# Kernel optimization log

Hardware: AMD Instinct MI355X
Metric: run time of the kernel (lower is better)

## Reference

```python
import jax, jax.numpy as jnp
import numpy as np

D = 1024
DK = 1024
B, S = 4, 2048

def setup_inputs() -> dict:
    key = jax.random.key(0)
    ks = jax.random.split(key, 7)
    x = jax.random.normal(ks[0], (B, S, D), dtype=jnp.float32)
    mask = jnp.zeros((B, S, S), dtype=jnp.float32)
    scale = 1.0 / np.sqrt(D)
    Wq = jax.random.normal(ks[1], (D, DK), dtype=jnp.float32) * scale
    bq = jax.random.normal(ks[2], (DK,), dtype=jnp.float32) * 0.01
    Wk = jax.random.normal(ks[3], (D, DK), dtype=jnp.float32) * scale
    bk = jax.random.normal(ks[4], (DK,), dtype=jnp.float32) * 0.01
    Wv = jax.random.normal(ks[5], (D, DK), dtype=jnp.float32) * scale
    bv = jax.random.normal(ks[6], (DK,), dtype=jnp.float32) * 0.01
    return {"x": x, "mask": mask, "Wq": Wq, "bq": bq, "Wk": Wk, "bk": bk, "Wv": Wv, "bv": bv}

def reference(x, mask, Wq, bq, Wk, bk, Wv, bv):
    # Q/K/V projections: [B,S,D] @ [D,DK] + bias -> [B,S,DK]
    Q = jnp.einsum('bsd,dk->bsk', x, Wq) + bq
    K = jnp.einsum('bsd,dk->bsk', x, Wk) + bk
    V = jnp.einsum('bsd,dk->bsk', x, Wv) + bv
    scale = 1.0 / jnp.sqrt(jnp.asarray(DK, dtype=Q.dtype))
    scores = jnp.einsum('bqk,bpk->bqp', Q, K) * scale + mask  # [B,S,S]
    attn = jax.nn.softmax(scores, axis=-1)
    return jnp.einsum('bqp,bpk->bqk', attn, V)
```

## Files before the change

### kernel.cpp

```cpp
#include <hip/hip_runtime.h>
#include <hip/hip_bf16.h>
#include <stdint.h>

typedef unsigned short u16;
typedef __attribute__((ext_vector_type(4))) unsigned short u16x4;
typedef __attribute__((ext_vector_type(8))) short short8;
typedef __attribute__((ext_vector_type(4))) float f32x4;

__device__ inline u16 f2b(float f) {
  uint32_t u = __builtin_bit_cast(uint32_t, f);
  u += 0x7fffu + ((u >> 16) & 1u);
  return (u16)(u >> 16);
}
__device__ inline float b2f(u16 b) {
  return __builtin_bit_cast(float, (uint32_t)b << 16);
}

__global__ __launch_bounds__(256) void prep(
    const float* __restrict__ x, u16* __restrict__ xb,
    const float* __restrict__ Wq, const float* __restrict__ Wk,
    const float* __restrict__ Wv, u16* __restrict__ wT,
    const float* __restrict__ bq, const float* __restrict__ bk,
    const float* __restrict__ bv, float* __restrict__ biasC,
    float* __restrict__ rowsum) {
  __shared__ float tl[32][33];
  const int b = blockIdx.x;
  const int t = threadIdx.x;
  if (b < 8192) {
    long i = ((long)b * 256 + t) * 4;
    float4 v = *(const float4*)(x + i);
    u16x4 o = { f2b(v.x), f2b(v.y), f2b(v.z), f2b(v.w) };
    *(u16x4*)(xb + i) = o;
  } else if (b < 8192 + 3072) {
    const int bb = b - 8192;
    const int z = bb >> 10;
    const int tile = bb & 1023;
    const float* in = z == 0 ? Wq : (z == 1 ? Wk : Wv);
    u16* o = wT + (long)z * 1024 * 1024;
    const int c0 = (tile & 31) * 32, r0 = (tile >> 5) * 32;
    const int tx = t & 31, ty = t >> 5;
#pragma unroll
    for (int j = 0; j < 32; j += 8)
      tl[ty + j][tx] = in[(long)(r0 + ty + j) * 1024 + c0 + tx];
    __syncthreads();
#pragma unroll
    for (int j = 0; j < 32; j += 8)
      o[(long)(c0 + ty + j) * 1024 + r0 + tx] = f2b(tl[tx][ty + j]);
  } else {
    const int i = (b - 8192 - 3072) * 256 + t;
    if (i < 3072)
      biasC[i] = i < 1024 ? bq[i] : (i < 2048 ? bk[i - 1024] : bv[i - 2048]);
    else if (i < 3072 + 8192)
      rowsum[i - 3072] = 0.0f;
  }
}

#define BM 128
#define BN 128
#define BK 64

__device__ inline void load_lds16(const void* g, void* l) {
  __builtin_amdgcn_global_load_lds((const __attribute__((address_space(1))) void*)g,
                                   (__attribute__((address_space(3))) void*)l, 16, 0, 0);
}

template <int MODE>
__global__ __launch_bounds__(256, 2) void gemm_bt(
    const u16* __restrict__ A, const u16* __restrict__ Bt, void* __restrict__ C,
    u16* __restrict__ vtOut,
    const float* __restrict__ bias, const float* __restrict__ rsum,
    const float* __restrict__ maskG,
    int K, int lda, int ldb, int ldc,
    long sA, long sB, long sC,
    float scale)
{
  const int z = blockIdx.z;
  A += z * sA;
  Bt += z * sB;
  const long cbase = z * sC;

  __shared__ __align__(16) u16 lA[BM * BK];
  __shared__ __align__(16) u16 lB[BN * BK];

  const int t = threadIdx.x;
  const int lane = t & 63;
  const int wave = t >> 6;
  const int wr = wave >> 1, wc = wave & 1;
  const int m0 = blockIdx.y * BM, n0 = blockIdx.x * BN;

  const int fr = lane & 15;
  const int q4 = lane >> 4;
  const int r0 = q4 * 4;

  float mpre[4][4][4];
  if (MODE == 2) {
    const float* mk = maskG + (long)z * 2048 * 2048;
#pragma unroll
    for (int i = 0; i < 4; i++)
#pragma unroll
      for (int j = 0; j < 4; j++) {
        const int row = m0 + wr * 64 + i * 16 + r0;
        const int col = n0 + wc * 64 + j * 16 + fr;
#pragma unroll
        for (int r = 0; r < 4; r++)
          mpre[i][j][r] = mk[(long)(row + r) * 2048 + col];
      }
#pragma unroll
    for (int i = 0; i < 4; i++)
#pragma unroll
      for (int j = 0; j < 4; j++)
#pragma unroll
        for (int r = 0; r < 4; r++)
          asm volatile("" : "+v"(mpre[i][j][r]));
  }

  const int srow = t >> 3;
  const int schunk = (t & 7) ^ (srow & 7);
  const u16* aS = A + (long)(m0 + srow) * lda + schunk * 8;
  const u16* bS = Bt + (long)(n0 + srow) * ldb + schunk * 8;

  f32x4 acc[4][4] = {};

  for (int k0 = 0; k0 < K; k0 += BK) {
    __syncthreads();
#pragma unroll
    for (int i = 0; i < 4; i++) {
      load_lds16(aS + k0 + (long)(i * 32) * lda, &lA[(i * 256 + t) * 8]);
      load_lds16(bS + k0 + (long)(i * 32) * ldb, &lB[(i * 256 + t) * 8]);
    }
    __syncthreads();
#pragma unroll
    for (int kk = 0; kk < 2; kk++) {
      const int ch = kk * 4 + q4;
      short8 aF[4], bF[4];
#pragma unroll
      for (int i = 0; i < 4; i++) {
        int row = wr * 64 + i * 16 + fr;
        aF[i] = *(const short8*)&lA[row * BK + ((ch ^ (row & 7)) * 8)];
      }
#pragma unroll
      for (int j = 0; j < 4; j++) {
        int row = wc * 64 + j * 16 + fr;
        bF[j] = *(const short8*)&lB[row * BK + ((ch ^ (row & 7)) * 8)];
      }
#pragma unroll
      for (int i = 0; i < 4; i++)
#pragma unroll
        for (int j = 0; j < 4; j++)
          acc[i][j] = __builtin_amdgcn_mfma_f32_16x16x32_bf16(aF[i], bF[j], acc[i][j], 0, 0, 0);
    }
  }

  if (MODE == 2) {
    u16* Pout = (u16*)C + cbase;
    float* rz = (float*)rsum + (long)z * 2048;
#pragma unroll
    for (int i = 0; i < 4; i++) {
      const int row = m0 + wr * 64 + i * 16 + r0;
      float rs[4] = {0.f, 0.f, 0.f, 0.f};
#pragma unroll
      for (int j = 0; j < 4; j++) {
        const int col = n0 + wc * 64 + j * 16 + fr;
#pragma unroll
        for (int r = 0; r < 4; r++) {
          float e = __expf(acc[i][j][r] * scale + mpre[i][j][r]);
          Pout[(long)(row + r) * ldc + col] = f2b(e);
          rs[r] += e;
        }
      }
#pragma unroll
      for (int r = 0; r < 4; r++) {
        float s = rs[r];
        s += __shfl_xor(s, 1); s += __shfl_xor(s, 2);
        s += __shfl_xor(s, 4); s += __shfl_xor(s, 8);
        if (fr == 0) atomicAdd(&rz[row + r], s);
      }
    }
  } else if (MODE == 0) {
#pragma unroll
    for (int i = 0; i < 4; i++) {
#pragma unroll
      for (int j = 0; j < 4; j++) {
        const int row = m0 + wr * 64 + i * 16 + r0;
        const int col = n0 + wc * 64 + j * 16 + fr;
        const float b = bias[col];
        if (col >= 2048) {
          u16x4 o = { f2b(acc[i][j][0] + b), f2b(acc[i][j][1] + b),
                      f2b(acc[i][j][2] + b), f2b(acc[i][j][3] + b) };
          *(u16x4*)(vtOut + (long)(col - 2048) * 8192 + row) = o;
        } else {
#pragma unroll
          for (int r = 0; r < 4; r++)
            ((u16*)C)[(long)(row + r) * ldc + col] = f2b(acc[i][j][r] + b);
        }
      }
    }
  } else {
    const float* lz = rsum + (long)z * 2048;
#pragma unroll
    for (int i = 0; i < 4; i++) {
      const int row = m0 + wr * 64 + i * 16 + r0;
      float inv[4];
#pragma unroll
      for (int r = 0; r < 4; r++) inv[r] = 1.0f / lz[row + r];
#pragma unroll
      for (int j = 0; j < 4; j++) {
        const int col = n0 + wc * 64 + j * 16 + fr;
#pragma unroll
        for (int r = 0; r < 4; r++)
          ((float*)C)[cbase + (long)(row + r) * ldc + col] = acc[i][j][r] * inv[r];
      }
    }
  }
}

extern "C" void kernel_launch(void* const* d_in, const int* in_sizes, int n_in,
                              void* d_out, int out_size, void* d_ws, size_t ws_size,
                              hipStream_t stream) {
  const float* x    = (const float*)d_in[0];
  const float* mask = (const float*)d_in[1];
  const float* Wq   = (const float*)d_in[2];
  const float* bq   = (const float*)d_in[3];
  const float* Wk   = (const float*)d_in[4];
  const float* bk   = (const float*)d_in[5];
  const float* Wv   = (const float*)d_in[6];
  const float* bv   = (const float*)d_in[7];
  float* out = (float*)d_out;

  char* w = (char*)d_ws;
  u16*   xb    = (u16*)(w);
  u16*   wT    = (u16*)(w + 16777216);
  float* biasC = (float*)(w + 23068672);
  u16*   QKV   = (u16*)(w + 23081088);
  u16*   Vt    = (u16*)(w + 73414016);
  u16*   Pp    = (u16*)(w + 90191232);
  float* rowsum= (float*)(w + 123745664);

  prep<<<8192 + 3072 + 44, 256, 0, stream>>>(x, xb, Wq, Wk, Wv, wT, bq, bk, bv, biasC, rowsum);

  gemm_bt<0><<<dim3(24, 64, 1), 256, 0, stream>>>(xb, wT, QKV, Vt, biasC, nullptr, nullptr,
      1024, 1024, 1024, 3072, 0, 0, 0, 1.0f);

  gemm_bt<2><<<dim3(16, 16, 4), 256, 0, stream>>>(QKV, QKV + 1024, Pp, nullptr, nullptr, rowsum,
      mask,
      1024, 3072, 3072, 2048,
      2048L * 3072, 2048L * 3072, 2048L * 2048, 0.03125f);

  gemm_bt<4><<<dim3(8, 16, 4), 256, 0, stream>>>(Pp, Vt, out, nullptr, nullptr, rowsum, nullptr,
      2048, 2048, 8192, 1024,
      2048L * 2048, 2048L, 2048L * 1024, 1.0f);
}
```

Before: 308.2 us.

## Use 256x256 double-buffered 8-wave GEMM with interleaved LDS prefetch for QKV and scores

Replaces the 128x128 single-buffered GEMM for the QKV projection and the QK^T scores with a 512-thread, 256x256-tile kernel. It double-buffers LDS and splits each K-tile into four quarter-stages, issuing global-to-LDS loads for the next tile while MFMAs run, with explicit barriers, waitcnts and setprio. The mask is now loaded in the epilogue instead of being prefetched into registers, which frees registers for the larger accumulator. The P·V GEMM keeps the old kernel. The larger tiles give fewer blocks (384 and 256), which risks underfilling the CUs, and the hand-written wait counts are fragile.

```diff
diff --git a/kernel.cpp b/kernel.cpp
--- a/kernel.cpp
+++ b/kernel.cpp
@@ -55,115 +55,151 @@
   }
 }
 
-#define BM 128
-#define BN 128
-#define BK 64
-
 __device__ inline void load_lds16(const void* g, void* l) {
   __builtin_amdgcn_global_load_lds((const __attribute__((address_space(1))) void*)g,
                                    (__attribute__((address_space(3))) void*)l, 16, 0, 0);
 }
 
+#define BAR  asm volatile("s_barrier" ::: "memory")
+#define LGK0 asm volatile("s_waitcnt lgkmcnt(0)" ::: "memory")
+#define VM4  asm volatile("s_waitcnt vmcnt(4)" ::: "memory")
+
+#define MM(IH, JH) do {                                                        \
+  __builtin_amdgcn_s_setprio(1);                                               \
+  _Pragma("unroll")                                                            \
+  for (int i_ = 0; i_ < 4; i_++)                                               \
+    _Pragma("unroll")                                                          \
+    for (int j_ = 0; j_ < 2; j_++)                                             \
+      _Pragma("unroll")                                                        \
+      for (int kk_ = 0; kk_ < 2; kk_++)                                        \
+        acc[(IH)*4 + i_][(JH)*2 + j_] = __builtin_amdgcn_mfma_f32_16x16x32_bf16( \
+            aF[i_][kk_], bF[j_][kk_], acc[(IH)*4 + i_][(JH)*2 + j_], 0, 0, 0); \
+  __builtin_amdgcn_s_setprio(0);                                               \
+} while (0)
+
 template <int MODE>
-__global__ __launch_bounds__(256, 2) void gemm_bt(
+__global__ __launch_bounds__(512, 1) void gemm8(
     const u16* __restrict__ A, const u16* __restrict__ Bt, void* __restrict__ C,
-    u16* __restrict__ vtOut,
-    const float* __restrict__ bias, const float* __restrict__ rsum,
-    const float* __restrict__ maskG,
+    u16* __restrict__ vtOut, const float* __restrict__ bias,
+    float* __restrict__ rsum, const float* __restrict__ maskG,
     int K, int lda, int ldb, int ldc,
-    long sA, long sB, long sC,
-    float scale)
+    long sA_, long sB_, long sC_, float scale)
 {
   const int z = blockIdx.z;
-  A += z * sA;
-  Bt += z * sB;
-  const long cbase = z * sC;
-
-  __shared__ __align__(16) u16 lA[BM * BK];
-  __shared__ __align__(16) u16 lB[BN * BK];
+  A += z * sA_;
+  Bt += z * sB_;
+  const long cbase = z * sC_;
+
+  __shared__ __align__(16) u16 sA[2][256 * 64];
+  __shared__ __align__(16) u16 sB[2][256 * 64];
 
   const int t = threadIdx.x;
-  const int lane = t & 63;
-  const int wave = t >> 6;
-  const int wr = wave >> 1, wc = wave & 1;
-  const int m0 = blockIdx.y * BM, n0 = blockIdx.x * BN;
-
-  const int fr = lane & 15;
-  const int q4 = lane >> 4;
-  const int r0 = q4 * 4;
-
-  float mpre[4][4][4];
+  const int lane = t & 63, wave = t >> 6;
+  const int wr = wave >> 2, wc = wave & 3;
+  const int fr = lane & 15, q4 = lane >> 4;
+  const int m0 = blockIdx.y * 256, n0 = blockIdx.x * 256;
+  const int nT = K / 64;
+
+  auto stA = [&](int half, int kt, int buf) {
+    if (kt >= nT) kt = 0;
+    const long ko = (long)kt * 64;
+#pragma unroll
+    for (int ii = 0; ii < 2; ii++) {
+      int c = ii * 512 + t;
+      int rr = c >> 3, slot = c & 7;
+      int row = (rr < 64) ? (half * 64 + rr) : (128 + half * 64 + rr - 64);
+      int gch = slot ^ (row & 7);
+      load_lds16(A + (long)(m0 + row) * lda + ko + gch * 8,
+                 &sA[buf][row * 64 + slot * 8]);
+    }
+  };
+  auto stB = [&](int half, int kt, int buf) {
+    if (kt >= nT) kt = 0;
+    const long ko = (long)kt * 64;
+#pragma unroll
+    for (int ii = 0; ii < 2; ii++) {
+      int c = ii * 512 + t;
+      int rr = c >> 3, slot = c & 7;
+      int row = (rr >> 5) * 64 + half * 32 + (rr & 31);
+      int gch = slot ^ (row & 7);
+      load_lds16(Bt + (long)(n0 + row) * ldb + ko + gch * 8,
+                 &sB[buf][row * 64 + slot * 8]);
+    }
+  };
+
+  short8 aF[4][2], bF[2][2];
+  f32x4 acc[8][4] = {};
+
+  auto rdA = [&](int half, int buf) {
+#pragma unroll
+    for (int i = 0; i < 4; i++) {
+      int row = wr * 128 + half * 64 + i * 16 + fr;
+#pragma unroll
+      for (int kk = 0; kk < 2; kk++) {
+        int ch = kk * 4 + q4;
+        aF[i][kk] = *(const short8*)&sA[buf][row * 64 + ((ch ^ (row & 7)) * 8)];
+      }
+    }
+  };
+  auto rdB = [&](int half, int buf) {
+#pragma unroll
+    for (int j = 0; j < 2; j++) {
+      int row = wc * 64 + half * 32 + j * 16 + fr;
+#pragma unroll
+      for (int kk = 0; kk < 2; kk++) {
+        int ch = kk * 4 + q4;
+        bF[j][kk] = *(const short8*)&sB[buf][row * 64 + ((ch ^ (row & 7)) * 8)];
+      }
+    }
+  };
+
+  stA(0, 0, 0); stB(0, 0, 0); stB(1, 0, 0); stA(1, 0, 0);
+  VM4; BAR;
+
+  const int nIt = nT / 2;
+#pragma unroll 1
+  for (int it = 0; it < nIt; ++it) {
+    const int kt = 2 * it;
+    rdA(0, 0); rdB(0, 0); stA(0, kt + 1, 1);
+    BAR; LGK0; MM(0, 0); VM4; BAR;
+    rdB(1, 0);            stB(0, kt + 1, 1);
+    BAR; LGK0; MM(0, 1); VM4; BAR;
+    rdA(1, 0);            stB(1, kt + 1, 1);
+    BAR; LGK0; MM(1, 1);      BAR;
+    rdB(0, 0);            stA(1, kt + 1, 1);
+    BAR; LGK0; MM(1, 0); VM4; BAR;
+    rdA(0, 1); rdB(0, 1); stA(0, kt + 2, 0);
+    BAR; LGK0; MM(0, 0); VM4; BAR;
+    rdB(1, 1);            stB(0, kt + 2, 0);
+    BAR; LGK0; MM(0, 1); VM4; BAR;
+    rdA(1, 1);            stB(1, kt + 2, 0);
+    BAR; LGK0; MM(1, 1);      BAR;
+    rdB(0, 1);            stA(1, kt + 2, 0);
+    BAR; LGK0; MM(1, 0); VM4; BAR;
+  }
+
   if (MODE == 2) {
     const float* mk = maskG + (long)z * 2048 * 2048;
-#pragma unroll
-    for (int i = 0; i < 4; i++)
-#pragma unroll
-      for (int j = 0; j < 4; j++) {
-        const int row = m0 + wr * 64 + i * 16 + r0;
-        const int col = n0 + wc * 64 + j * 16 + fr;
-#pragma unroll
-        for (int r = 0; r < 4; r++)
-          mpre[i][j][r] = mk[(long)(row + r) * 2048 + col];
-      }
-#pragma unroll
-    for (int i = 0; i < 4; i++)
-#pragma unroll
-      for (int j = 0; j < 4; j++)
-#pragma unroll
-        for (int r = 0; r < 4; r++)
-          asm volatile("" : "+v"(mpre[i][j][r]));
-  }
-
-  const int srow = t >> 3;
-  const int schunk = (t & 7) ^ (srow & 7);
-  const u16* aS = A + (long)(m0 + srow) * lda + schunk * 8;
-  const u16* bS = Bt + (long)(n0 + srow) * ldb + schunk * 8;
-
-  f32x4 acc[4][4] = {};
-
-  for (int k0 = 0; k0 < K; k0 += BK) {
-    __syncthreads();
-#pragma unroll
-    for (int i = 0; i < 4; i++) {
-      load_lds16(aS + k0 + (long)(i * 32) * lda, &lA[(i * 256 + t) * 8]);
-      load_lds16(bS + k0 + (long)(i * 32) * ldb, &lB[(i * 256 + t) * 8]);
-    }
-    __syncthreads();
-#pragma unroll
-    for (int kk = 0; kk < 2; kk++) {
-      const int ch = kk * 4 + q4;
-      short8 aF[4], bF[4];
-#pragma unroll
-      for (int i = 0; i < 4; i++) {
-        int row = wr * 64 + i * 16 + fr;
-        aF[i] = *(const short8*)&lA[row * BK + ((ch ^ (row & 7)) * 8)];
-      }
-#pragma unroll
-      for (int j = 0; j < 4; j++) {
-        int row = wc * 64 + j * 16 + fr;
-        bF[j] = *(const short8*)&lB[row * BK + ((ch ^ (row & 7)) * 8)];
-      }
-#pragma unroll
-      for (int i = 0; i < 4; i++)
-#pragma unroll
-        for (int j = 0; j < 4; j++)
-          acc[i][j] = __builtin_amdgcn_mfma_f32_16x16x32_bf16(aF[i], bF[j], acc[i][j], 0, 0, 0);
-    }
-  }
-
-  if (MODE == 2) {
     u16* Pout = (u16*)C + cbase;
-    float* rz = (float*)rsum + (long)z * 2048;
-#pragma unroll
-    for (int i = 0; i < 4; i++) {
-      const int row = m0 + wr * 64 + i * 16 + r0;
-      float rs[4] = {0.f, 0.f, 0.f, 0.f};
+    float* rz = rsum + (long)z * 2048;
+#pragma unroll
+    for (int i = 0; i < 8; i++) {
+      const int row = m0 + wr * 128 + i * 16 + q4 * 4;
+      float ml[4][4];
 #pragma unroll
       for (int j = 0; j < 4; j++) {
         const int col = n0 + wc * 64 + j * 16 + fr;
 #pragma unroll
+        for (int r = 0; r < 4; r++)
+          ml[j][r] = mk[(long)(row + r) * 2048 + col];
+      }
+      float rs[4] = {0.f, 0.f, 0.f, 0.f};
+#pragma unroll
+      for (int j = 0; j < 4; j++) {
+        const int col = n0 + wc * 64 + j * 16 + fr;
+#pragma unroll
         for (int r = 0; r < 4; r++) {
-          float e = __expf(acc[i][j][r] * scale + mpre[i][j][r]);
+          float e = __expf(acc[i][j][r] * scale + ml[j][r]);
           Pout[(long)(row + r) * ldc + col] = f2b(e);
           rs[r] += e;
         }
@@ -176,12 +212,12 @@
         if (fr == 0) atomicAdd(&rz[row + r], s);
       }
     }
-  } else if (MODE == 0) {
-#pragma unroll
-    for (int i = 0; i < 4; i++) {
+  } else {
+#pragma unroll
+    for (int i = 0; i < 8; i++) {
 #pragma unroll
       for (int j = 0; j < 4; j++) {
-        const int row = m0 + wr * 64 + i * 16 + r0;
+        const int row = m0 + wr * 128 + i * 16 + q4 * 4;
         const int col = n0 + wc * 64 + j * 16 + fr;
         const float b = bias[col];
         if (col >= 2048) {
@@ -195,21 +231,85 @@
         }
       }
     }
-  } else {
-    const float* lz = rsum + (long)z * 2048;
+  }
+}
+
+#define BM 128
+#define BN 128
+#define BK 64
+
+__global__ __launch_bounds__(256, 2) void gemm_pv(
+    const u16* __restrict__ A, const u16* __restrict__ Bt, float* __restrict__ C,
+    const float* __restrict__ rsum,
+    int K, int lda, int ldb, int ldc, long sA_, long sB_, long sC_)
+{
+  const int z = blockIdx.z;
+  A += z * sA_;
+  Bt += z * sB_;
+  const long cbase = z * sC_;
+
+  __shared__ __align__(16) u16 lA[BM * BK];
+  __shared__ __align__(16) u16 lB[BN * BK];
+
+  const int t = threadIdx.x;
+  const int lane = t & 63;
+  const int wave = t >> 6;
+  const int wr = wave >> 1, wc = wave & 1;
+  const int m0 = blockIdx.y * BM, n0 = blockIdx.x * BN;
+
+  const int srow = t >> 3;
+  const int schunk = (t & 7) ^ (srow & 7);
+  const u16* aS = A + (long)(m0 + srow) * lda + schunk * 8;
+  const u16* bS = Bt + (long)(n0 + srow) * ldb + schunk * 8;
+
+  f32x4 acc[4][4] = {};
+  const int fr = lane & 15;
+  const int q4 = lane >> 4;
+
+  for (int k0 = 0; k0 < K; k0 += BK) {
+    __syncthreads();
 #pragma unroll
     for (int i = 0; i < 4; i++) {
-      const int row = m0 + wr * 64 + i * 16 + r0;
-      float inv[4];
-#pragma unroll
-      for (int r = 0; r < 4; r++) inv[r] = 1.0f / lz[row + r];
+      load_lds16(aS + k0 + (long)(i * 32) * lda, &lA[(i * 256 + t) * 8]);
+      load_lds16(bS + k0 + (long)(i * 32) * ldb, &lB[(i * 256 + t) * 8]);
+    }
+    __syncthreads();
+#pragma unroll
+    for (int kk = 0; kk < 2; kk++) {
+      const int ch = kk * 4 + q4;
+      short8 aF[4], bF[4];
+#pragma unroll
+      for (int i = 0; i < 4; i++) {
+        int row = wr * 64 + i * 16 + fr;
+        aF[i] = *(const short8*)&lA[row * BK + ((ch ^ (row & 7)) * 8)];
+      }
 #pragma unroll
       for (int j = 0; j < 4; j++) {
-        const int col = n0 + wc * 64 + j * 16 + fr;
-#pragma unroll
-        for (int r = 0; r < 4; r++)
-          ((float*)C)[cbase + (long)(row + r) * ldc + col] = acc[i][j][r] * inv[r];
-      }
+        int row = wc * 64 + j * 16 + fr;
+        bF[j] = *(const short8*)&lB[row * BK + ((ch ^ (row & 7)) * 8)];
+      }
+#pragma unroll
+      for (int i = 0; i < 4; i++)
+#pragma unroll
+        for (int j = 0; j < 4; j++)
+          acc[i][j] = __builtin_amdgcn_mfma_f32_16x16x32_bf16(aF[i], bF[j], acc[i][j], 0, 0, 0);
+    }
+  }
+
+  const int r0 = q4 * 4;
+  const float* lz = rsum + (long)z * 2048;
+#pragma unroll
+  for (int i = 0; i < 4; i++) {
+    const int row = m0 + wr * 64 + i * 16 + r0;
+    float inv[4];
+#pragma unroll
+    for (int r = 0; r < 4; r++) inv[r] = 1.0f / lz[row + r];
+#pragma unroll
+    for (int j = 0; j < 4; j++) {
+      const int col = n0 + wc * 64 + j * 16 + fr;
+#pragma unroll
+      for (int r = 0; r < 4; r++)
+        C[cbase + (long)(row + r) * ldc + col] = acc[i][j][r] * inv[r];
     }
   }
 }
@@ -238,15 +338,15 @@
 
   prep<<<8192 + 3072 + 44, 256, 0, stream>>>(x, xb, Wq, Wk, Wv, wT, bq, bk, bv, biasC, rowsum);
 
-  gemm_bt<0><<<dim3(24, 64, 1), 256, 0, stream>>>(xb, wT, QKV, Vt, biasC, nullptr, nullptr,
+  gemm8<0><<<dim3(12, 32, 1), 512, 0, stream>>>(xb, wT, QKV, Vt, biasC, nullptr, nullptr,
       1024, 1024, 1024, 3072, 0, 0, 0, 1.0f);
 
-  gemm_bt<2><<<dim3(16, 16, 4), 256, 0, stream>>>(QKV, QKV + 1024, Pp, nullptr, nullptr, rowsum,
+  gemm8<2><<<dim3(8, 8, 4), 512, 0, stream>>>(QKV, QKV + 1024, Pp, nullptr, nullptr, rowsum,
       mask,
       1024, 3072, 3072, 2048,
       2048L * 3072, 2048L * 3072, 2048L * 2048, 0.03125f);
 
-  gemm_bt<4><<<dim3(8, 16, 4), 256, 0, stream>>>(Pp, Vt, out, nullptr, nullptr, rowsum, nullptr,
+  gemm_pv<<<dim3(8, 16, 4), 256, 0, stream>>>(Pp, Vt, out, rowsum,
       2048, 2048, 8192, 1024,
-      2048L * 2048, 2048L, 2048L * 1024, 1.0f);
-}
+      2048L * 2048, 2048L, 2048L * 1024);
+}
```

New measurement: 313.2 us. About the same (+1.6%).

## Fuse prep and three GEMM stages into one persistent kernel with grid barriers

Applied to the files above, without the earlier changes.

Replaces the four separate launches (prep, QKV projection, score+exp, PV) with a single persistent kernel of 512 blocks. Blocks loop over each stage's tiles and synchronise through atomic-counter grid barriers, with a memset to reset the counters. Mask loading in the score stage moves from a register prefetch before the GEMM loop to per-row loads in the epilogue. This removes launch gaps and frees registers, but adds barrier spin cost and makes tiles run in fixed waves, so stages whose tile count does not divide evenly by 512 leave some blocks idle.

```diff
diff --git a/kernel.cpp b/kernel.cpp
--- a/kernel.cpp
+++ b/kernel.cpp
@@ -12,107 +12,42 @@
   u += 0x7fffu + ((u >> 16) & 1u);
   return (u16)(u >> 16);
 }
-__device__ inline float b2f(u16 b) {
-  return __builtin_bit_cast(float, (uint32_t)b << 16);
-}
-
-__global__ __launch_bounds__(256) void prep(
-    const float* __restrict__ x, u16* __restrict__ xb,
-    const float* __restrict__ Wq, const float* __restrict__ Wk,
-    const float* __restrict__ Wv, u16* __restrict__ wT,
-    const float* __restrict__ bq, const float* __restrict__ bk,
-    const float* __restrict__ bv, float* __restrict__ biasC,
-    float* __restrict__ rowsum) {
-  __shared__ float tl[32][33];
-  const int b = blockIdx.x;
-  const int t = threadIdx.x;
-  if (b < 8192) {
-    long i = ((long)b * 256 + t) * 4;
-    float4 v = *(const float4*)(x + i);
-    u16x4 o = { f2b(v.x), f2b(v.y), f2b(v.z), f2b(v.w) };
-    *(u16x4*)(xb + i) = o;
-  } else if (b < 8192 + 3072) {
-    const int bb = b - 8192;
-    const int z = bb >> 10;
-    const int tile = bb & 1023;
-    const float* in = z == 0 ? Wq : (z == 1 ? Wk : Wv);
-    u16* o = wT + (long)z * 1024 * 1024;
-    const int c0 = (tile & 31) * 32, r0 = (tile >> 5) * 32;
-    const int tx = t & 31, ty = t >> 5;
-#pragma unroll
-    for (int j = 0; j < 32; j += 8)
-      tl[ty + j][tx] = in[(long)(r0 + ty + j) * 1024 + c0 + tx];
-    __syncthreads();
-#pragma unroll
-    for (int j = 0; j < 32; j += 8)
-      o[(long)(c0 + ty + j) * 1024 + r0 + tx] = f2b(tl[tx][ty + j]);
-  } else {
-    const int i = (b - 8192 - 3072) * 256 + t;
-    if (i < 3072)
-      biasC[i] = i < 1024 ? bq[i] : (i < 2048 ? bk[i - 1024] : bv[i - 2048]);
-    else if (i < 3072 + 8192)
-      rowsum[i - 3072] = 0.0f;
-  }
-}
 
 #define BM 128
 #define BN 128
 #define BK 64
+#define NBLK 512
 
 __device__ inline void load_lds16(const void* g, void* l) {
   __builtin_amdgcn_global_load_lds((const __attribute__((address_space(1))) void*)g,
                                    (__attribute__((address_space(3))) void*)l, 16, 0, 0);
 }
 
+__device__ inline void gbar(int* cnt) {
+  __syncthreads();
+  if (threadIdx.x == 0) {
+    __threadfence();
+    __hip_atomic_fetch_add(cnt, 1, __ATOMIC_ACQ_REL, __HIP_MEMORY_SCOPE_AGENT);
+    while (__hip_atomic_load(cnt, __ATOMIC_ACQUIRE, __HIP_MEMORY_SCOPE_AGENT) < NBLK)
+      __builtin_amdgcn_s_sleep(2);
+  }
+  __syncthreads();
+  __threadfence();
+}
+
 template <int MODE>
-__global__ __launch_bounds__(256, 2) void gemm_bt(
+__device__ __forceinline__ void gemm_tile(
+    u16* lA, u16* lB,
     const u16* __restrict__ A, const u16* __restrict__ Bt, void* __restrict__ C,
-    u16* __restrict__ vtOut,
-    const float* __restrict__ bias, const float* __restrict__ rsum,
-    const float* __restrict__ maskG,
+    u16* __restrict__ vtOut, const float* __restrict__ bias,
+    float* __restrict__ rsum, const float* __restrict__ maskG,
     int K, int lda, int ldb, int ldc,
-    long sA, long sB, long sC,
-    float scale)
+    int m0, int n0, long cbase, int z, float scale)
 {
-  const int z = blockIdx.z;
-  A += z * sA;
-  Bt += z * sB;
-  const long cbase = z * sC;
-
-  __shared__ __align__(16) u16 lA[BM * BK];
-  __shared__ __align__(16) u16 lB[BN * BK];
-
   const int t = threadIdx.x;
   const int lane = t & 63;
   const int wave = t >> 6;
   const int wr = wave >> 1, wc = wave & 1;
-  const int m0 = blockIdx.y * BM, n0 = blockIdx.x * BN;
-
-  const int fr = lane & 15;
-  const int q4 = lane >> 4;
-  const int r0 = q4 * 4;
-
-  float mpre[4][4][4];
-  if (MODE == 2) {
-    const float* mk = maskG + (long)z * 2048 * 2048;
-#pragma unroll
-    for (int i = 0; i < 4; i++)
-#pragma unroll
-      for (int j = 0; j < 4; j++) {
-        const int row = m0 + wr * 64 + i * 16 + r0;
-        const int col = n0 + wc * 64 + j * 16 + fr;
-#pragma unroll
-        for (int r = 0; r < 4; r++)
-          mpre[i][j][r] = mk[(long)(row + r) * 2048 + col];
-      }
-#pragma unroll
-    for (int i = 0; i < 4; i++)
-#pragma unroll
-      for (int j = 0; j < 4; j++)
-#pragma unroll
-        for (int r = 0; r < 4; r++)
-          asm volatile("" : "+v"(mpre[i][j][r]));
-  }
 
   const int srow = t >> 3;
   const int schunk = (t & 7) ^ (srow & 7);
@@ -120,6 +55,8 @@
   const u16* bS = Bt + (long)(n0 + srow) * ldb + schunk * 8;
 
   f32x4 acc[4][4] = {};
+  const int fr = lane & 15;
+  const int q4 = lane >> 4;
 
   for (int k0 = 0; k0 < K; k0 += BK) {
     __syncthreads();
@@ -151,19 +88,29 @@
     }
   }
 
+  const int r0 = q4 * 4;
   if (MODE == 2) {
+    const float* mk = maskG + (long)z * 2048 * 2048;
     u16* Pout = (u16*)C + cbase;
-    float* rz = (float*)rsum + (long)z * 2048;
+    float* rz = rsum + (long)z * 2048;
 #pragma unroll
     for (int i = 0; i < 4; i++) {
       const int row = m0 + wr * 64 + i * 16 + r0;
+      float ml[4][4];
+#pragma unroll
+      for (int j = 0; j < 4; j++) {
+        const int col = n0 + wc * 64 + j * 16 + fr;
+#pragma unroll
+        for (int r = 0; r < 4; r++)
+          ml[j][r] = mk[(long)(row + r) * 2048 + col];
+      }
       float rs[4] = {0.f, 0.f, 0.f, 0.f};
 #pragma unroll
       for (int j = 0; j < 4; j++) {
         const int col = n0 + wc * 64 + j * 16 + fr;
 #pragma unroll
         for (int r = 0; r < 4; r++) {
-          float e = __expf(acc[i][j][r] * scale + mpre[i][j][r]);
+          float e = __expf(acc[i][j][r] * scale + ml[j][r]);
           Pout[(long)(row + r) * ldc + col] = f2b(e);
           rs[r] += e;
         }
@@ -211,6 +158,83 @@
           ((float*)C)[cbase + (long)(row + r) * ldc + col] = acc[i][j][r] * inv[r];
       }
     }
+  }
+}
+
+__global__ __launch_bounds__(256, 2) void fused(
+    const float* __restrict__ x, const float* __restrict__ mask,
+    const float* __restrict__ Wq, const float* __restrict__ Wk,
+    const float* __restrict__ Wv,
+    const float* __restrict__ bq, const float* __restrict__ bk,
+    const float* __restrict__ bv,
+    u16* xb, u16* wT, float* biasC,
+    u16* QKV, u16* Vt, u16* Pp,
+    float* rowsum, int* bar, float* out)
+{
+  __shared__ __align__(16) u16 lA[BM * BK];
+  __shared__ __align__(16) u16 lB[BN * BK];
+  const int t = threadIdx.x;
+
+  for (int b = blockIdx.x; b < 8192 + 3072 + 44; b += NBLK) {
+    if (b < 8192) {
+      long i = ((long)b * 256 + t) * 4;
+      float4 v = *(const float4*)(x + i);
+      u16x4 o = { f2b(v.x), f2b(v.y), f2b(v.z), f2b(v.w) };
+      *(u16x4*)(xb + i) = o;
+    } else if (b < 8192 + 3072) {
+      float* tl = (float*)lA;
+      const int bb = b - 8192;
+      const int zz = bb >> 10;
+      const int tile = bb & 1023;
+      const float* in = zz == 0 ? Wq : (zz == 1 ? Wk : Wv);
+      u16* o = wT + (long)zz * 1024 * 1024;
+      const int c0 = (tile & 31) * 32, r0 = (tile >> 5) * 32;
+      const int tx = t & 31, ty = t >> 5;
+      __syncthreads();
+#pragma unroll
+      for (int j = 0; j < 32; j += 8)
+        tl[(ty + j) * 33 + tx] = in[(long)(r0 + ty + j) * 1024 + c0 + tx];
+      __syncthreads();
+#pragma unroll
+      for (int j = 0; j < 32; j += 8)
+        o[(long)(c0 + ty + j) * 1024 + r0 + tx] = f2b(tl[tx * 33 + ty + j]);
+    } else {
+      const int i = (b - 8192 - 3072) * 256 + t;
+      if (i < 3072)
+        biasC[i] = i < 1024 ? bq[i] : (i < 2048 ? bk[i - 1024] : bv[i - 2048]);
+      else if (i < 3072 + 8192)
+        rowsum[i - 3072] = 0.0f;
+    }
+  }
+  gbar(&bar[0]);
+
+  for (int idx = blockIdx.x; idx < 1536; idx += NBLK) {
+    const int bx = idx % 24, by = idx / 24;
+    gemm_tile<0>(lA, lB, xb, wT, QKV, Vt, biasC, nullptr, nullptr,
+                 1024, 1024, 1024, 3072, by * BM, bx * BN, 0, 0, 1.0f);
+  }
+  gbar(&bar[1]);
+
+  for (int idx = blockIdx.x; idx < 1024; idx += NBLK) {
+    const int zz = idx >> 8, rem = idx & 255;
+    const int bx = rem & 15, by = rem >> 4;
+    gemm_tile<2>(lA, lB,
+                 QKV + (long)zz * 2048 * 3072, QKV + 1024 + (long)zz * 2048 * 3072,
+                 Pp, nullptr, nullptr, rowsum, mask,
+                 1024, 3072, 3072, 2048, by * BM, bx * BN,
+                 (long)zz * 2048 * 2048, zz, 0.03125f);
+  }
+  gbar(&bar[2]);
+
+  {
+    const int idx = blockIdx.x;
+    const int zz = idx >> 7, rem = idx & 127;
+    const int bx = rem & 7, by = rem >> 3;
+    gemm_tile<4>(lA, lB,
+                 Pp + (long)zz * 2048 * 2048, Vt + (long)zz * 2048,
+                 out, nullptr, nullptr, rowsum, nullptr,
+                 2048, 2048, 8192, 1024, by * BM, bx * BN,
+                 (long)zz * 2048 * 1024, zz, 1.0f);
   }
 }
 
@@ -235,18 +259,9 @@
   u16*   Vt    = (u16*)(w + 73414016);
   u16*   Pp    = (u16*)(w + 90191232);
   float* rowsum= (float*)(w + 123745664);
-
-  prep<<<8192 + 3072 + 44, 256, 0, stream>>>(x, xb, Wq, Wk, Wv, wT, bq, bk, bv, biasC, rowsum);
-
-  gemm_bt<0><<<dim3(24, 64, 1), 256, 0, stream>>>(xb, wT, QKV, Vt, biasC, nullptr, nullptr,
-      1024, 1024, 1024, 3072, 0, 0, 0, 1.0f);
-
-  gemm_bt<2><<<dim3(16, 16, 4), 256, 0, stream>>>(QKV, QKV + 1024, Pp, nullptr, nullptr, rowsum,
-      mask,
-      1024, 3072, 3072, 2048,
-      2048L * 3072, 2048L * 3072, 2048L * 2048, 0.03125f);
-
-  gemm_bt<4><<<dim3(8, 16, 4), 256, 0, stream>>>(Pp, Vt, out, nullptr, nullptr, rowsum, nullptr,
-      2048, 2048, 8192, 1024,
-      2048L * 2048, 2048L, 2048L * 1024, 1.0f);
-}
+  int*   bar   = (int*)(w + 123778432);
+
+  hipMemsetAsync(bar, 0, 3 * sizeof(int), stream);
+  fused<<<NBLK, 256, 0, stream>>>(x, mask, Wq, Wk, Wv, bq, bk, bv,
+                                  xb, wT, biasC, QKV, Vt, Pp, rowsum, bar, out);
+}
```

Measured after the change: 609.4 us. +97.7%, slower.
